# Performance work log

Hardware: AMD Instinct MI355X
Metric: run time of the kernel (lower is better)

## Reference

```python
import jax, jax.numpy as jnp
import numpy as np

B, S, H, FF, E = 4, 4096, 1024, 4096, 8
EPS = 1e-5


def setup_inputs() -> dict:
    key = jax.random.key(0)
    ks = jax.random.split(key, 8)
    std = 0.02
    return {
        "x": jax.random.normal(ks[0], (B, S, H), jnp.float32),
        "norm_weight": jnp.ones((H,), jnp.float32),
        "router_w": jax.random.normal(ks[1], (E, H), jnp.float32) * std,
        "router_b": jnp.zeros((E,), jnp.float32),
        "fc1_w": jax.random.normal(ks[2], (E, FF, H), jnp.float32) * std,
        "fc1_b": jnp.zeros((E, FF), jnp.float32),
        "fc2_w": jax.random.normal(ks[3], (E, H, FF), jnp.float32) * std,
        "fc2_b": jnp.zeros((E, H), jnp.float32),
    }


def reference(x, norm_weight, router_w, router_b, fc1_w, fc1_b, fc2_w, fc2_b):
    b, s, h = x.shape
    T = b * s
    e = router_w.shape[0]
    cap = T // e  # expert capacity, capacity_factor = 1.0

    x_flat = x.reshape(T, h)
    # RMSNorm (pre-norm on MoE input)
    xn = x_flat * jax.lax.rsqrt(jnp.mean(x_flat * x_flat, axis=-1, keepdims=True) + EPS) * norm_weight

    # Router (no jitter: eval / jitter_noise=0)
    logits = xn @ router_w.T + router_b          # [T, E]
    probs = jax.nn.softmax(logits, axis=-1)       # [T, E]

    # Expert-choice routing: each expert picks its top-`cap` tokens by prob
    gates, idx = jax.lax.top_k(probs.T, cap)      # [E, cap], [E, cap]

    # Dispatch (gather) and grouped expert MLP
    xe = xn[idx]                                   # [E, cap, H]
    hmid = jnp.einsum('ech,efh->ecf', xe, fc1_w) + fc1_b[:, None, :]
    hmid = jax.nn.gelu(hmid, approximate=False)    # torch F.gelu default (exact)
    ye = jnp.einsum('ecf,ehf->ech', hmid, fc2_w) + fc2_b[:, None, :]

    # Combine: gated scatter-add back to token positions, normalize by gate sum
    flat_idx = idx.reshape(-1)                     # [E*cap]
    weighted = (ye * gates[..., None]).reshape(-1, h)
    out = jnp.zeros((T, h), x.dtype).at[flat_idx].add(weighted)
    gate_sums = jnp.zeros((T, 1), x.dtype).at[flat_idx].add(gates.reshape(-1, 1))
    out = out / jnp.maximum(gate_sums, 1e-9)       # unrouted tokens stay zero
    return out.reshape(b, s, h)
```

## Files before the change

kernel.cpp:

```cpp
#include <hip/hip_runtime.h>
#include <hip/hip_bf16.h>

#define T_TOK 16384
#define H_DIM 1024
#define FF_DIM 4096
#define NE 8
#define CAP 2048
#define EPS_F 1e-5f

#define BM2 256
#define BN2 256
#define BK2 32

typedef __attribute__((ext_vector_type(4))) float f32x4;
typedef __attribute__((ext_vector_type(8))) short bf16x8;
typedef unsigned long long u64;
typedef unsigned int u32;

__device__ inline void gload_lds16(const void* g, void* l) {
  __builtin_amdgcn_global_load_lds(
      (const __attribute__((address_space(1))) unsigned int*)g,
      (__attribute__((address_space(3))) unsigned int*)l, 16, 0, 0);
}

__device__ inline unsigned short bf16_bits(float f) {
  __hip_bfloat16 h = __float2bfloat16(f);
  unsigned short u;
  __builtin_memcpy(&u, &h, 2);
  return u;
}

__device__ inline float bits_f32(unsigned short u) {
  const u32 x = ((u32)u) << 16;
  float f;
  __builtin_memcpy(&f, &x, 4);
  return f;
}

__global__ __launch_bounds__(256) void router_kernel(
    const float* __restrict__ x, const float* __restrict__ nw,
    const float* __restrict__ rw, const float* __restrict__ rb,
    __hip_bfloat16* __restrict__ xn, u64* __restrict__ keys) {
  const int t = blockIdx.x;
  const int tid = threadIdx.x;
  const float4 v = reinterpret_cast<const float4*>(x + (size_t)t * H_DIM)[tid];
  float ss = v.x * v.x + v.y * v.y + v.z * v.z + v.w * v.w;
#pragma unroll
  for (int o = 32; o > 0; o >>= 1) ss += __shfl_down(ss, o);
  __shared__ float red[4];
  __shared__ float redl[4][NE];
  const int wv = tid >> 6, ln = tid & 63;
  if (ln == 0) red[wv] = ss;
  __syncthreads();
  const float tot = red[0] + red[1] + red[2] + red[3];
  const float scale = rsqrtf(tot * (1.0f / H_DIM) + EPS_F);
  const float4 w4 = reinterpret_cast<const float4*>(nw)[tid];
  float xv0 = v.x * scale * w4.x, xv1 = v.y * scale * w4.y;
  float xv2 = v.z * scale * w4.z, xv3 = v.w * scale * w4.w;
  ushort4 u4;
  u4.x = bf16_bits(xv0); u4.y = bf16_bits(xv1);
  u4.z = bf16_bits(xv2); u4.w = bf16_bits(xv3);
  reinterpret_cast<ushort4*>(xn + (size_t)t * H_DIM)[tid] = u4;
  float lg[NE];
#pragma unroll
  for (int e = 0; e < NE; ++e) {
    const float4 r4 = reinterpret_cast<const float4*>(rw + (size_t)e * H_DIM)[tid];
    lg[e] = xv0 * r4.x + xv1 * r4.y + xv2 * r4.z + xv3 * r4.w;
  }
#pragma unroll
  for (int o = 32; o > 0; o >>= 1) {
#pragma unroll
    for (int e = 0; e < NE; ++e) lg[e] += __shfl_down(lg[e], o);
  }
  if (ln == 0) {
#pragma unroll
    for (int e = 0; e < NE; ++e) redl[wv][e] = lg[e];
  }
  __syncthreads();
  if (tid == 0) {
    float l[NE];
    float m = -1e30f;
#pragma unroll
    for (int e = 0; e < NE; ++e) {
      l[e] = redl[0][e] + redl[1][e] + redl[2][e] + redl[3][e] + rb[e];
      m = fmaxf(m, l[e]);
    }
    float s = 0.f;
#pragma unroll
    for (int e = 0; e < NE; ++e) { l[e] = expf(l[e] - m); s += l[e]; }
    const float inv = 1.0f / s;
#pragma unroll
    for (int e = 0; e < NE; ++e) {
      const float p = l[e] * inv;
      const u64 key = ((u64)__float_as_uint(p) << 32) | (u32)(0xFFFFFFFFu - (u32)t);
      keys[(size_t)e * T_TOK + t] = key;
    }
  }
}

__global__ __launch_bounds__(1024) void topk_kernel(
    const u64* __restrict__ keys, int* __restrict__ idxl,
    float* __restrict__ gatel, int* __restrict__ tok_list, int* __restrict__ tok_cnt) {
  const int e = blockIdx.x;
  const int tid = threadIdx.x;
  const int lane = tid & 63;
  const u64* ke = keys + (size_t)e * T_TOK;
  __shared__ int hist[256];
  __shared__ u64 s_pref;
  __shared__ int s_k;
  __shared__ int s_cnt;
  u64 pref = 0;
  int pbits = 0;
  int kneed = CAP;
  for (int pass = 0; pass < 8; ++pass) {
    if (tid < 256) hist[tid] = 0;
    __syncthreads();
    const int shift = 56 - 8 * pass;
    for (int i = tid; i < T_TOK; i += 1024) {
      const u64 key = ke[i];
      const bool ok = (pbits == 0) || ((key >> (64 - pbits)) == pref);
      const int d = ok ? (int)((key >> shift) & 255) : -1;
      u64 act = __ballot(ok);
      while (act) {
        const int src = __ffsll((long long)act) - 1;
        const int dl = __shfl(d, src);
        const u64 mb = __ballot(ok && (d == dl));
        if (lane == src) atomicAdd(&hist[dl], (int)__popcll(mb));
        act &= ~mb;
      }
    }
    __syncthreads();
    if (tid == 0) {
      int cum = 0;
      int d = 255;
      for (; d >= 0; --d) {
        cum += hist[d];
        if (cum >= kneed) break;
      }
      s_k = kneed - (cum - hist[d]);
      s_pref = (pref << 8) | (u64)(u32)d;
    }
    __syncthreads();
    pref = s_pref;
    kneed = s_k;
    pbits += 8;
    __syncthreads();
  }
  if (tid == 0) s_cnt = 0;
  __syncthreads();
  for (int i = tid; i < T_TOK; i += 1024) {
    const u64 key = ke[i];
    if (key >= pref) {
      const int pos = atomicAdd(&s_cnt, 1);
      if (pos < CAP) {
        const int tok = (int)(0xFFFFFFFFu - (u32)(key & 0xFFFFFFFFu));
        const float p = __uint_as_float((u32)(key >> 32));
        idxl[e * CAP + pos] = tok;
        gatel[e * CAP + pos] = p;
        const int j = atomicAdd(tok_cnt + tok, 1);
        if (j < NE) tok_list[tok * NE + j] = e * CAP + pos;
      }
    }
  }
}

__global__ __launch_bounds__(256) void cvt2_kernel(
    const float* __restrict__ s1, __hip_bfloat16* __restrict__ d1,
    const float* __restrict__ s2, __hip_bfloat16* __restrict__ d2, int n4each) {
  int i = blockIdx.x * blockDim.x + threadIdx.x;
  const int stride = gridDim.x * blockDim.x;
  for (; i < 2 * n4each; i += stride) {
    const float* s = (i < n4each) ? s1 : s2;
    __hip_bfloat16* d = (i < n4each) ? d1 : d2;
    const int j = (i < n4each) ? i : i - n4each;
    const float4 v = reinterpret_cast<const float4*>(s)[j];
    ushort4 o;
    o.x = bf16_bits(v.x); o.y = bf16_bits(v.y);
    o.z = bf16_bits(v.z); o.w = bf16_bits(v.w);
    reinterpret_cast<ushort4*>(d)[j] = o;
  }
}

template <int MODE>
__global__ __launch_bounds__(512, 2) void gemm6_kernel(
    const __hip_bfloat16* __restrict__ Asrc, const __hip_bfloat16* __restrict__ Bw,
    const float* __restrict__ bias, const int* __restrict__ idxl,
    const float* __restrict__ gatel, __hip_bfloat16* __restrict__ hmid,
    __hip_bfloat16* __restrict__ ye, int ebase) {
  constexpr int N = (MODE == 0) ? FF_DIM : H_DIM;
  constexpr int K = (MODE == 0) ? H_DIM : FF_DIM;
  constexpr int NBN = N / BN2;
  constexpr int LOG_NBN = (MODE == 0) ? 4 : 2;
  constexpr int BPE = (CAP / BM2) * NBN;
  constexpr int LOG_BPE = (MODE == 0) ? 7 : 5;
  constexpr int NT = K / BK2;

  const int nwg = gridDim.x;
  const int wg0 = blockIdx.x;
  const int wg = (wg0 & 7) * (nwg >> 3) + (wg0 >> 3);
  const int z = wg >> LOG_BPE;
  const int rr = wg & (BPE - 1);
  const int bm = rr >> LOG_NBN;
  const int bn = rr & (NBN - 1);
  const int e = ebase + z;

  const int tid = threadIdx.x;
  const int lane = tid & 63;
  const int w = tid >> 6;
  const int wr = w >> 2, wc = w & 3;
  const int fr = lane & 15, q = lane >> 4;

  __shared__ char smem[131072];

  const int srow = tid >> 2;
  const int sg = tid & 3;
  const int skoff = (sg ^ ((srow >> 1) & 3)) * 8;

  const __hip_bfloat16* asrc0;
  const __hip_bfloat16* asrc1;
  if constexpr (MODE == 0) {
    const int t0 = idxl[e * CAP + bm * BM2 + srow];
    const int t1 = idxl[e * CAP + bm * BM2 + 128 + srow];
    asrc0 = Asrc + (size_t)t0 * H_DIM + skoff;
    asrc1 = Asrc + (size_t)t1 * H_DIM + skoff;
  } else {
    asrc0 = Asrc + ((size_t)z * CAP + bm * BM2 + srow) * FF_DIM + skoff;
    asrc1 = asrc0 + (size_t)128 * FF_DIM;
  }
  const __hip_bfloat16* bsrc0 = Bw + (size_t)z * N * K + (size_t)(bn * BN2 + srow) * K + skoff;
  const __hip_bfloat16* bsrc1 = bsrc0 + (size_t)128 * K;

  const int slotk = ((q ^ ((fr >> 1) & 3)) << 4);
  int aoff[8], boff[4];
#pragma unroll
  for (int m = 0; m < 8; ++m) aoff[m] = (wr * 128 + m * 16 + fr) * 64 + slotk;
#pragma unroll
  for (int n = 0; n < 4; ++n) boff[n] = 16384 + (wc * 64 + n * 16 + fr) * 64 + slotk;

  f32x4 acc[8][4] = {};
  bf16x8 Aa[4], Ab[4], B0f[2], B1f[2];

#define GLDA(sb, k0)                                             \
  do {                                                           \
    char* d_ = smem + (sb)*32768 + tid * 16;                     \
    gload_lds16(asrc0 + (k0), d_);                               \
    gload_lds16(asrc1 + (k0), d_ + 8192);                        \
  } while (0)
#define GLDB(sb, k0)                                             \
  do {                                                           \
    char* d_ = smem + (sb)*32768 + tid * 16;                     \
    gload_lds16(bsrc0 + (k0), d_ + 16384);                       \
    gload_lds16(bsrc1 + (k0), d_ + 24576);                       \
  } while (0)

  GLDA(0, 0); GLDB(0, 0);
  GLDA(1, BK2); GLDB(1, BK2);
  GLDA(2, 2 * BK2); GLDB(2, 2 * BK2);
  asm volatile("s_waitcnt vmcnt(4)");
  __builtin_amdgcn_s_barrier();
  __builtin_amdgcn_sched_barrier(0);

  for (int kt = 0; kt < NT; ++kt) {
    const int cur = kt & 3;
    const int kref = (kt + 3 < NT) ? (kt + 3) : (kt + 3 - NT);
    const int k0p = kref * BK2;
    const int psl = (kt + 3) & 3;
    const char* base = smem + cur * 32768;

    Aa[0] = *reinterpret_cast<const bf16x8*>(base + aoff[0]);
    Aa[1] = *reinterpret_cast<const bf16x8*>(base + aoff[1]);
    Aa[2] = *reinterpret_cast<const bf16x8*>(base + aoff[2]);
    Aa[3] = *reinterpret_cast<const bf16x8*>(base + aoff[3]);
    B0f[0] = *reinterpret_cast<const bf16x8*>(base + boff[0]);
    B0f[1] = *reinterpret_cast<const bf16x8*>(base + boff[1]);
    B1f[0] = *reinterpret_cast<const bf16x8*>(base + boff[2]);
    B1f[1] = *reinterpret_cast<const bf16x8*>(base + boff[3]);
    __builtin_amdgcn_sched_barrier(0);
    Ab[0] = *reinterpret_cast<const bf16x8*>(base + aoff[4]);
    Ab[1] = *reinterpret_cast<const bf16x8*>(base + aoff[5]);
    Ab[2] = *reinterpret_cast<const bf16x8*>(base + aoff[6]);
    Ab[3] = *reinterpret_cast<const bf16x8*>(base + aoff[7]);
    GLDA(psl, k0p);
    asm volatile("s_waitcnt vmcnt(6)");
    __builtin_amdgcn_s_barrier();
    asm volatile("s_waitcnt lgkmcnt(4)");
    __builtin_amdgcn_sched_barrier(0);
    __builtin_amdgcn_s_setprio(1);
#pragma unroll
    for (int m_ = 0; m_ < 4; ++m_) {
      acc[m_][0] = __builtin_amdgcn_mfma_f32_16x16x32_bf16(Aa[m_], B0f[0], acc[m_][0], 0, 0, 0);
      acc[m_][1] = __builtin_amdgcn_mfma_f32_16x16x32_bf16(Aa[m_], B0f[1], acc[m_][1], 0, 0, 0);
      acc[m_][2] = __builtin_amdgcn_mfma_f32_16x16x32_bf16(Aa[m_], B1f[0], acc[m_][2], 0, 0, 0);
      acc[m_][3] = __builtin_amdgcn_mfma_f32_16x16x32_bf16(Aa[m_], B1f[1], acc[m_][3], 0, 0, 0);
    }
    __builtin_amdgcn_s_setprio(0);
    __builtin_amdgcn_sched_barrier(0);

    GLDB(psl, k0p);
    asm volatile("s_waitcnt lgkmcnt(0)");
    __builtin_amdgcn_sched_barrier(0);
    __builtin_amdgcn_s_barrier();
    __builtin_amdgcn_sched_barrier(0);
    __builtin_amdgcn_s_setprio(1);
#pragma unroll
    for (int m_ = 0; m_ < 4; ++m_) {
      acc[4 + m_][0] = __builtin_amdgcn_mfma_f32_16x16x32_bf16(Ab[m_], B0f[0], acc[4 + m_][0], 0, 0, 0);
      acc[4 + m_][1] = __builtin_amdgcn_mfma_f32_16x16x32_bf16(Ab[m_], B0f[1], acc[4 + m_][1], 0, 0, 0);
      acc[4 + m_][2] = __builtin_amdgcn_mfma_f32_16x16x32_bf16(Ab[m_], B1f[0], acc[4 + m_][2], 0, 0, 0);
      acc[4 + m_][3] = __builtin_amdgcn_mfma_f32_16x16x32_bf16(Ab[m_], B1f[1], acc[4 + m_][3], 0, 0, 0);
    }
    __builtin_amdgcn_s_setprio(0);
    __builtin_amdgcn_sched_barrier(0);
  }
#undef GLDA
#undef GLDB

  if constexpr (MODE == 0) {
#pragma unroll
    for (int m = 0; m < 8; ++m) {
      const int rbase = bm * BM2 + wr * 128 + m * 16 + q * 4;
#pragma unroll
      for (int n = 0; n < 4; ++n) {
        const int gn = bn * BN2 + wc * 64 + n * 16 + fr;
        const float bb = bias[e * FF_DIM + gn];
#pragma unroll
        for (int i = 0; i < 4; ++i) {
          const float v = acc[m][n][i] + bb;
          const float u = v * (1.5957691216f + 0.0713548162972f * v * v);
          const float s = 1.0f / (1.0f + __expf(-u));
          hmid[((size_t)z * CAP + rbase + i) * FF_DIM + gn] = __float2bfloat16(v * s);
        }
      }
    }
  } else {
#pragma unroll
    for (int m = 0; m < 8; ++m) {
      const int rbase = bm * BM2 + wr * 128 + m * 16 + q * 4;
      float gt[4];
#pragma unroll
      for (int i = 0; i < 4; ++i) gt[i] = gatel[e * CAP + rbase + i];
#pragma unroll
      for (int n = 0; n < 4; ++n) {
        const int gn = bn * BN2 + wc * 64 + n * 16 + fr;
        const float bb = bias[e * H_DIM + gn];
#pragma unroll
        for (int i = 0; i < 4; ++i)
          ye[((size_t)e * CAP + rbase + i) * H_DIM + gn] =
              __float2bfloat16((acc[m][n][i] + bb) * gt[i]);
      }
    }
  }
}

__global__ __launch_bounds__(256) void combine_kernel(
    const __hip_bfloat16* __restrict__ ye, const float* __restrict__ gatel,
    const int* __restrict__ tok_list, const int* __restrict__ tok_cnt,
    float* __restrict__ out) {
  const int t = blockIdx.x;
  const int tid = threadIdx.x;
  const int cnt = tok_cnt[t];
  float a0 = 0.f, a1 = 0.f, a2 = 0.f, a3 = 0.f, gs = 0.f;
  for (int j = 0; j < cnt && j < NE; ++j) {
    const int ent = tok_list[t * NE + j];
    gs += gatel[ent];
    const ushort4 v = reinterpret_cast<const ushort4*>(ye + (size_t)ent * H_DIM)[tid];
    a0 += bits_f32(v.x);
    a1 += bits_f32(v.y);
    a2 += bits_f32(v.z);
    a3 += bits_f32(v.w);
  }
  const float inv = 1.0f / fmaxf(gs, 1e-9f);
  float4 o;
  o.x = a0 * inv; o.y = a1 * inv; o.z = a2 * inv; o.w = a3 * inv;
  reinterpret_cast<float4*>(out + (size_t)t * H_DIM)[tid] = o;
}

extern "C" void kernel_launch(void* const* d_in, const int* in_sizes, int n_in,
                              void* d_out, int out_size, void* d_ws, size_t ws_size,
                              hipStream_t stream) {
  const float* x = (const float*)d_in[0];
  const float* nw = (const float*)d_in[1];
  const float* rw = (const float*)d_in[2];
  const float* rb = (const float*)d_in[3];
  const float* fc1w = (const float*)d_in[4];
  const float* fc1b = (const float*)d_in[5];
  const float* fc2w = (const float*)d_in[6];
  const float* fc2b = (const float*)d_in[7];
  float* out = (float*)d_out;

  char* ws = (char*)d_ws;
  size_t off = 0;
  auto alloc = [&](size_t b) {
    char* p = ws + off;
    off += (b + 255) & ~(size_t)255;
    return p;
  };
  __hip_bfloat16* xn = (__hip_bfloat16*)alloc((size_t)T_TOK * H_DIM * 2);
  u64* keys = (u64*)alloc((size_t)NE * T_TOK * 8);
  int* idxl = (int*)alloc((size_t)NE * CAP * 4);
  float* gatel = (float*)alloc((size_t)NE * CAP * 4);
  int* tok_list = (int*)alloc((size_t)T_TOK * NE * 4);
  int* tok_cnt = (int*)alloc((size_t)T_TOK * 4);
  __hip_bfloat16* ye = (__hip_bfloat16*)alloc((size_t)NE * CAP * H_DIM * 2);

  int EC = NE;
  while (EC > 1) {
    const size_t per = (size_t)EC * ((size_t)FF_DIM * H_DIM * 2 * 2 + (size_t)CAP * FF_DIM * 2);
    if (off + per + 4096 <= ws_size) break;
    EC >>= 1;
  }
  __hip_bfloat16* w1b = (__hip_bfloat16*)alloc((size_t)EC * FF_DIM * H_DIM * 2);
  __hip_bfloat16* w2b = (__hip_bfloat16*)alloc((size_t)EC * H_DIM * FF_DIM * 2);
  __hip_bfloat16* hmid = (__hip_bfloat16*)alloc((size_t)EC * CAP * FF_DIM * 2);

  hipMemsetAsync(tok_cnt, 0, (size_t)T_TOK * 4, stream);

  router_kernel<<<T_TOK, 256, 0, stream>>>(x, nw, rw, rb, xn, keys);
  topk_kernel<<<NE, 1024, 0, stream>>>(keys, idxl, gatel, tok_list, tok_cnt);

  for (int eb = 0; eb < NE; eb += EC) {
    const int n4 = EC * FF_DIM * H_DIM / 4;
    cvt2_kernel<<<4096, 256, 0, stream>>>(fc1w + (size_t)eb * FF_DIM * H_DIM, w1b,
                                          fc2w + (size_t)eb * H_DIM * FF_DIM, w2b, n4);
    const int nb1 = EC * (CAP / BM2) * (FF_DIM / BN2);
    gemm6_kernel<0><<<nb1, 512, 0, stream>>>(xn, w1b, fc1b, idxl, gatel, hmid, ye, eb);
    const int nb2 = EC * (CAP / BM2) * (H_DIM / BN2);
    gemm6_kernel<1><<<nb2, 512, 0, stream>>>(hmid, w2b, fc2b, idxl, gatel, hmid, ye, eb);
  }
  combine_kernel<<<T_TOK, 256, 0, stream>>>(ye, gatel, tok_list, tok_cnt, out);
}
```

Before: 547.8 us.

## Use 1024-thread workgroups with 16 waves each computing a 64x64 subtile

The 256x256 GEMM tile is now computed by 16 waves (1024 threads) instead of 8. Each wave owns a 64x64 subtile with half the accumulators, and each thread issues one global-to-LDS load per operand per stage. The aim is to cut per-wave register pressure and add waves to hide latency. In exchange it drops the launch bound that allowed two workgroups per CU, adds barrier overhead across more waves, and lowers the ratio of MFMA work to LDS reads per wave.

```diff
diff --git a/kernel.cpp b/kernel.cpp
--- a/kernel.cpp
+++ b/kernel.cpp
@@ -182,7 +182,7 @@
 }
 
 template <int MODE>
-__global__ __launch_bounds__(512, 2) void gemm6_kernel(
+__global__ __launch_bounds__(1024) void gemm7_kernel(
     const __hip_bfloat16* __restrict__ Asrc, const __hip_bfloat16* __restrict__ Bw,
     const float* __restrict__ bias, const int* __restrict__ idxl,
     const float* __restrict__ gatel, __hip_bfloat16* __restrict__ hmid,
@@ -216,42 +216,24 @@
   const int sg = tid & 3;
   const int skoff = (sg ^ ((srow >> 1) & 3)) * 8;
 
-  const __hip_bfloat16* asrc0;
-  const __hip_bfloat16* asrc1;
+  const __hip_bfloat16* asrc;
   if constexpr (MODE == 0) {
     const int t0 = idxl[e * CAP + bm * BM2 + srow];
-    const int t1 = idxl[e * CAP + bm * BM2 + 128 + srow];
-    asrc0 = Asrc + (size_t)t0 * H_DIM + skoff;
-    asrc1 = Asrc + (size_t)t1 * H_DIM + skoff;
+    asrc = Asrc + (size_t)t0 * H_DIM + skoff;
   } else {
-    asrc0 = Asrc + ((size_t)z * CAP + bm * BM2 + srow) * FF_DIM + skoff;
-    asrc1 = asrc0 + (size_t)128 * FF_DIM;
-  }
-  const __hip_bfloat16* bsrc0 = Bw + (size_t)z * N * K + (size_t)(bn * BN2 + srow) * K + skoff;
-  const __hip_bfloat16* bsrc1 = bsrc0 + (size_t)128 * K;
+    asrc = Asrc + ((size_t)z * CAP + bm * BM2 + srow) * FF_DIM + skoff;
+  }
+  const __hip_bfloat16* bsrc = Bw + (size_t)z * N * K + (size_t)(bn * BN2 + srow) * K + skoff;
 
   const int slotk = ((q ^ ((fr >> 1) & 3)) << 4);
-  int aoff[8], boff[4];
-#pragma unroll
-  for (int m = 0; m < 8; ++m) aoff[m] = (wr * 128 + m * 16 + fr) * 64 + slotk;
-#pragma unroll
-  for (int n = 0; n < 4; ++n) boff[n] = 16384 + (wc * 64 + n * 16 + fr) * 64 + slotk;
-
-  f32x4 acc[8][4] = {};
-  bf16x8 Aa[4], Ab[4], B0f[2], B1f[2];
-
-#define GLDA(sb, k0)                                             \
-  do {                                                           \
-    char* d_ = smem + (sb)*32768 + tid * 16;                     \
-    gload_lds16(asrc0 + (k0), d_);                               \
-    gload_lds16(asrc1 + (k0), d_ + 8192);                        \
-  } while (0)
-#define GLDB(sb, k0)                                             \
-  do {                                                           \
-    char* d_ = smem + (sb)*32768 + tid * 16;                     \
-    gload_lds16(bsrc0 + (k0), d_ + 16384);                       \
-    gload_lds16(bsrc1 + (k0), d_ + 24576);                       \
-  } while (0)
+  const int aoff0 = (wr * 64 + fr) * 64 + slotk;
+  const int boff0 = 16384 + (wc * 64 + fr) * 64 + slotk;
+
+  f32x4 acc[4][4] = {};
+  bf16x8 Af[4], Bf[4];
+
+#define GLDA(sb, k0) gload_lds16(asrc + (k0), smem + (sb)*32768 + tid * 16)
+#define GLDB(sb, k0) gload_lds16(bsrc + (k0), smem + (sb)*32768 + 16384 + tid * 16)
 
   GLDA(0, 0); GLDB(0, 0);
   GLDA(1, BK2); GLDB(1, BK2);
@@ -267,31 +249,25 @@
     const int psl = (kt + 3) & 3;
     const char* base = smem + cur * 32768;
 
-    Aa[0] = *reinterpret_cast<const bf16x8*>(base + aoff[0]);
-    Aa[1] = *reinterpret_cast<const bf16x8*>(base + aoff[1]);
-    Aa[2] = *reinterpret_cast<const bf16x8*>(base + aoff[2]);
-    Aa[3] = *reinterpret_cast<const bf16x8*>(base + aoff[3]);
-    B0f[0] = *reinterpret_cast<const bf16x8*>(base + boff[0]);
-    B0f[1] = *reinterpret_cast<const bf16x8*>(base + boff[1]);
-    B1f[0] = *reinterpret_cast<const bf16x8*>(base + boff[2]);
-    B1f[1] = *reinterpret_cast<const bf16x8*>(base + boff[3]);
-    __builtin_amdgcn_sched_barrier(0);
-    Ab[0] = *reinterpret_cast<const bf16x8*>(base + aoff[4]);
-    Ab[1] = *reinterpret_cast<const bf16x8*>(base + aoff[5]);
-    Ab[2] = *reinterpret_cast<const bf16x8*>(base + aoff[6]);
-    Ab[3] = *reinterpret_cast<const bf16x8*>(base + aoff[7]);
+    Af[0] = *reinterpret_cast<const bf16x8*>(base + aoff0);
+    Af[1] = *reinterpret_cast<const bf16x8*>(base + aoff0 + 1024);
+    Af[2] = *reinterpret_cast<const bf16x8*>(base + aoff0 + 2048);
+    Af[3] = *reinterpret_cast<const bf16x8*>(base + aoff0 + 3072);
+    Bf[0] = *reinterpret_cast<const bf16x8*>(base + boff0);
+    Bf[1] = *reinterpret_cast<const bf16x8*>(base + boff0 + 1024);
+    __builtin_amdgcn_sched_barrier(0);
+    Bf[2] = *reinterpret_cast<const bf16x8*>(base + boff0 + 2048);
+    Bf[3] = *reinterpret_cast<const bf16x8*>(base + boff0 + 3072);
     GLDA(psl, k0p);
-    asm volatile("s_waitcnt vmcnt(6)");
+    asm volatile("s_waitcnt vmcnt(3)");
     __builtin_amdgcn_s_barrier();
-    asm volatile("s_waitcnt lgkmcnt(4)");
+    asm volatile("s_waitcnt lgkmcnt(2)");
     __builtin_amdgcn_sched_barrier(0);
     __builtin_amdgcn_s_setprio(1);
 #pragma unroll
     for (int m_ = 0; m_ < 4; ++m_) {
-      acc[m_][0] = __builtin_amdgcn_mfma_f32_16x16x32_bf16(Aa[m_], B0f[0], acc[m_][0], 0, 0, 0);
-      acc[m_][1] = __builtin_amdgcn_mfma_f32_16x16x32_bf16(Aa[m_], B0f[1], acc[m_][1], 0, 0, 0);
-      acc[m_][2] = __builtin_amdgcn_mfma_f32_16x16x32_bf16(Aa[m_], B1f[0], acc[m_][2], 0, 0, 0);
-      acc[m_][3] = __builtin_amdgcn_mfma_f32_16x16x32_bf16(Aa[m_], B1f[1], acc[m_][3], 0, 0, 0);
+      acc[m_][0] = __builtin_amdgcn_mfma_f32_16x16x32_bf16(Af[m_], Bf[0], acc[m_][0], 0, 0, 0);
+      acc[m_][1] = __builtin_amdgcn_mfma_f32_16x16x32_bf16(Af[m_], Bf[1], acc[m_][1], 0, 0, 0);
     }
     __builtin_amdgcn_s_setprio(0);
     __builtin_amdgcn_sched_barrier(0);
@@ -304,10 +280,8 @@
     __builtin_amdgcn_s_setprio(1);
 #pragma unroll
     for (int m_ = 0; m_ < 4; ++m_) {
-      acc[4 + m_][0] = __builtin_amdgcn_mfma_f32_16x16x32_bf16(Ab[m_], B0f[0], acc[4 + m_][0], 0, 0, 0);
-      acc[4 + m_][1] = __builtin_amdgcn_mfma_f32_16x16x32_bf16(Ab[m_], B0f[1], acc[4 + m_][1], 0, 0, 0);
-      acc[4 + m_][2] = __builtin_amdgcn_mfma_f32_16x16x32_bf16(Ab[m_], B1f[0], acc[4 + m_][2], 0, 0, 0);
-      acc[4 + m_][3] = __builtin_amdgcn_mfma_f32_16x16x32_bf16(Ab[m_], B1f[1], acc[4 + m_][3], 0, 0, 0);
+      acc[m_][2] = __builtin_amdgcn_mfma_f32_16x16x32_bf16(Af[m_], Bf[2], acc[m_][2], 0, 0, 0);
+      acc[m_][3] = __builtin_amdgcn_mfma_f32_16x16x32_bf16(Af[m_], Bf[3], acc[m_][3], 0, 0, 0);
     }
     __builtin_amdgcn_s_setprio(0);
     __builtin_amdgcn_sched_barrier(0);
@@ -317,8 +291,8 @@
 
   if constexpr (MODE == 0) {
 #pragma unroll
-    for (int m = 0; m < 8; ++m) {
-      const int rbase = bm * BM2 + wr * 128 + m * 16 + q * 4;
+    for (int m = 0; m < 4; ++m) {
+      const int rbase = bm * BM2 + wr * 64 + m * 16 + q * 4;
 #pragma unroll
       for (int n = 0; n < 4; ++n) {
         const int gn = bn * BN2 + wc * 64 + n * 16 + fr;
@@ -334,8 +308,8 @@
     }
   } else {
 #pragma unroll
-    for (int m = 0; m < 8; ++m) {
-      const int rbase = bm * BM2 + wr * 128 + m * 16 + q * 4;
+    for (int m = 0; m < 4; ++m) {
+      const int rbase = bm * BM2 + wr * 64 + m * 16 + q * 4;
       float gt[4];
 #pragma unroll
       for (int i = 0; i < 4; ++i) gt[i] = gatel[e * CAP + rbase + i];
@@ -423,9 +397,9 @@
     cvt2_kernel<<<4096, 256, 0, stream>>>(fc1w + (size_t)eb * FF_DIM * H_DIM, w1b,
                                           fc2w + (size_t)eb * H_DIM * FF_DIM, w2b, n4);
     const int nb1 = EC * (CAP / BM2) * (FF_DIM / BN2);
-    gemm6_kernel<0><<<nb1, 512, 0, stream>>>(xn, w1b, fc1b, idxl, gatel, hmid, ye, eb);
+    gemm7_kernel<0><<<nb1, 1024, 0, stream>>>(xn, w1b, fc1b, idxl, gatel, hmid, ye, eb);
     const int nb2 = EC * (CAP / BM2) * (H_DIM / BN2);
-    gemm6_kernel<1><<<nb2, 512, 0, stream>>>(hmid, w2b, fc2b, idxl, gatel, hmid, ye, eb);
+    gemm7_kernel<1><<<nb2, 1024, 0, stream>>>(hmid, w2b, fc2b, idxl, gatel, hmid, ye, eb);
   }
   combine_kernel<<<T_TOK, 256, 0, stream>>>(ye, gatel, tok_list, tok_cnt, out);
 }
```

Measured after the change: 545.6 us. No clear change (-0.4%).
